# Kernel optimization log

Hardware: AMD Instinct MI355X
Metric: run time of the kernel (lower is better)

Reference implementation:

```python
import jax, jax.numpy as jnp
import numpy as np

B, C, H, W = 256, 512, 14, 14
HW = H * W
TAU = 0.03          # args.tau
EPS = 0.65          # args.epsilon
EPS2 = 0.40         # args.epsilon - args.epsilon_margin
T_LOGIT = 0.07      # args.logit_temperature
MAX_ITERS = 32      # static unrolled bound for the data-dependent while-loop
PD_EPS = 1e-6       # torch.nn.PairwiseDistance default eps (added to the difference)


def setup_inputs() -> dict:
    key = jax.random.key(0)
    k1, k2 = jax.random.split(key)
    img = jax.random.normal(k1, (B, C, H, W), jnp.float32)
    img = img / (jnp.linalg.norm(img, axis=1, keepdims=True) + 1e-12)  # L2 over channels
    aud = jax.random.normal(k2, (B, C), jnp.float32)
    aud = aud / (jnp.linalg.norm(aud, axis=1, keepdims=True) + 1e-12)
    return {"img": img, "aud": aud}


def reference(img, aud):
    Bb, Cc, Hh, Ww = img.shape
    n_pix = Hh * Ww

    # PosLogits: [B,1,H,W]; Alllogits: [B,B,H,W]
    pos_logits = jnp.einsum('ncqa,nc->nqa', img, aud)[:, None]
    all_logits = jnp.einsum('ncqa,kc->nkqa', img, aud)

    # trimap negatives
    pos2 = jax.nn.sigmoid((pos_logits - EPS2) / TAU)
    neg = 1.0 - pos2                                        # [B,1,H,W]

    logit = img.reshape(Bb, Cc, -1) * pos_logits.reshape(Bb, 1, -1)   # [B,C,HW]
    positive0 = pos_logits.reshape(Bb, -1)                            # [B,HW]
    neg_val = (logit * neg.reshape(Bb, 1, -1)).mean(axis=2)           # [B,C]

    logit_t = logit.transpose(0, 2, 1)                                 # [B,HW,C]
    dist_to_zero = jnp.linalg.norm(logit_t - neg_val[:, None, :] + PD_EPS, axis=-1)  # [B,HW]

    def body(t, state):
        positive, already_pos, endpoint, obj = state
        idx = jnp.argmax(positive, axis=1)                             # [B] (detached in torch)
        sel = jnp.take_along_axis(logit, idx[:, None, None], axis=2)[:, :, 0]  # [B,C]
        obj = obj.at[t].set(sel * (~endpoint)[:, None].astype(sel.dtype))
        dist_to_logit = jnp.linalg.norm(logit_t - sel[:, None, :] + PD_EPS, axis=-1)  # [B,HW]
        pos = (dist_to_logit < dist_to_zero) & (~already_pos)
        already_pos = already_pos | pos
        positive = positive * (1.0 - pos.astype(positive.dtype))
        endpoint = endpoint | (pos.sum(axis=1) == 0) | (positive.max(axis=1) < 0.1)
        return (positive, already_pos, endpoint, obj)

    obj0 = jnp.zeros((MAX_ITERS, Bb, Cc), img.dtype)
    state0 = (positive0,
              jnp.zeros((Bb, n_pix), bool),
              jnp.zeros((Bb,), bool),
              obj0)
    _, _, _, object_arr = jax.lax.fori_loop(0, MAX_ITERS, body, state0)

    # lvs contrastive loss
    mask = 1.0 - 100.0 * jnp.eye(Bb, dtype=img.dtype)
    pos_m = jax.nn.sigmoid((pos_logits - EPS) / TAU)                   # [B,1,H,W]
    pos_all = jax.nn.sigmoid((all_logits - EPS) / TAU)                 # [B,B,H,W]
    sim1 = (pos_m * pos_logits).reshape(Bb, 1, -1).sum(-1) / pos_m.reshape(Bb, 1, -1).sum(-1)
    sim = (pos_all * all_logits).reshape(Bb, Bb, -1).sum(-1) / pos_all.reshape(Bb, Bb, -1).sum(-1) * mask
    sim2 = (neg * pos_logits).reshape(Bb, 1, -1).sum(-1) / neg.reshape(Bb, 1, -1).sum(-1)
    logits = jnp.concatenate((sim1, sim, sim2), axis=1) / T_LOGIT      # [B, B+2]
    loss = -jax.nn.log_softmax(logits, axis=1)[:, 0].mean()           # CE with target 0

    return loss, pos_logits[:, 0], object_arr
```

## Files before the change

kernel.cpp:

```cpp
#include <hip/hip_runtime.h>
#include <hip/hip_bf16.h>
#include <math.h>

#define NB 256
#define NC 512
#define NP 196
#define NIT 32
#define PROWS 208
#define LSTR 72
#define SFSTR 211

typedef __attribute__((ext_vector_type(8))) short bf16x8;
typedef __attribute__((ext_vector_type(4))) float f32x4;

__device__ __forceinline__ float sigf(float z){ return 1.0f/(1.0f+expf(-z)); }

__device__ __forceinline__ unsigned short f2bf(float x){
  return __bfloat16_as_ushort(__float2bfloat16(x));
}
__device__ __forceinline__ float bf2f(unsigned short h){
  union{float f; unsigned u;} v; v.u = ((unsigned)h)<<16; return v.f;
}
__device__ __forceinline__ double dshfl_xor(double v, int m){
  int lo = __shfl_xor(__double2loint(v), m);
  int hi = __shfl_xor(__double2hiint(v), m);
  return __hiloint2double(hi, lo);
}

__global__ __launch_bounds__(256) void aud2bf_kernel(const float* __restrict__ aud, unsigned short* __restrict__ aud_bf)
{
  int i = blockIdx.x*256 + threadIdx.x;
  aud_bf[i] = f2bf(aud[i]);
}


__global__ __launch_bounds__(512) void convert5_kernel(
    const float* __restrict__ img, const float* __restrict__ aud,
    unsigned short* __restrict__ pan,
    double* __restrict__ ppl, double* __restrict__ pcs)
{
  const int bid = blockIdx.x;
  const int b = bid & 255, part = bid >> 8;
  const int tid = threadIdx.x;
  const float* imgb = img + (size_t)b*NC*NP + (size_t)part*64*NP;
  __shared__ float sf[64*SFSTR];
  __shared__ float s_aud[64];
  if (tid < 64) s_aud[tid] = aud[b*NC + part*64 + tid];

  for (int j=tid; j<64*49; j+=512){
    int p4 = j % 49, c = j / 49;
    float4 v = *(const float4*)&imgb[(size_t)c*NP + p4*4];
    sf[c*SFSTR + p4*4+0]=v.x; sf[c*SFSTR + p4*4+1]=v.y;
    sf[c*SFSTR + p4*4+2]=v.z; sf[c*SFSTR + p4*4+3]=v.w;
  }
  __syncthreads();

  unsigned short* pp = pan + (size_t)(b*8+part)*PROWS*128;
  for (int j=tid; j<PROWS*8; j+=512){
    int p = j>>3, o = j&7;
    unsigned hw[4], lw[4];
    double dot=0.0, sm=0.0;
    #pragma unroll
    for (int k2=0;k2<4;++k2){
      int c = o*8 + 2*k2;
      float x0 = (p<NP) ? sf[c*SFSTR + p]     : 0.f;
      float x1 = (p<NP) ? sf[(c+1)*SFSTR + p] : 0.f;
      unsigned short h0=f2bf(x0), h1=f2bf(x1);
      unsigned short l0=f2bf(x0-bf2f(h0)), l1=f2bf(x1-bf2f(h1));
      hw[k2] = (unsigned)h0 | ((unsigned)h1<<16);
      lw[k2] = (unsigned)l0 | ((unsigned)l1<<16);
      dot += (double)x0*(double)s_aud[c] + (double)x1*(double)s_aud[c+1];
      sm  += (double)x0 + (double)x1;
    }
    *(uint4*)&pp[p*128 + o*8]      = *(uint4*)hw;
    *(uint4*)&pp[p*128 + 64 + o*8] = *(uint4*)lw;
    dot += dshfl_xor(dot,1); dot += dshfl_xor(dot,2); dot += dshfl_xor(dot,4);
    sm  += dshfl_xor(sm,1);  sm  += dshfl_xor(sm,2);  sm  += dshfl_xor(sm,4);
    if (o==0 && p<NP){
      ppl[(size_t)(b*8+part)*NP + p] = dot;
      pcs[(size_t)(b*8+part)*NP + p] = sm;
    }
  }
}

__global__ __launch_bounds__(256) void prep3_kernel(
    const double* __restrict__ ppl, const double* __restrict__ pcs,
    float* __restrict__ pl, float* __restrict__ cs,
    float* __restrict__ sim1, float* __restrict__ sim2, float* __restrict__ out_pl)
{
  const int b = blockIdx.x, tid = threadIdx.x;
  __shared__ double s_redd[256];
  float plv=0.f;
  if (tid < NP){
    double a=0.0, s=0.0;
    #pragma unroll
    for (int part=0; part<8; ++part){
      a += ppl[(size_t)(b*8+part)*NP + tid];
      s += pcs[(size_t)(b*8+part)*NP + tid];
    }
    plv=(float)a;
    float csv=(float)s;
    pl[b*NP+tid]=plv; cs[b*NP+tid]=csv; out_pl[b*NP+tid]=plv;
  }
  float pmw = (tid<NP)? sigf((plv-0.65f)/0.03f) : 0.f;
  float negw= (tid<NP)? 1.0f - sigf((plv-0.40f)/0.03f) : 0.f;
  double r[4];
  r[0]=(tid<NP)?(double)pmw*(double)plv:0.0;
  r[1]=(tid<NP)?(double)pmw:0.0;
  r[2]=(tid<NP)?(double)negw*(double)plv:0.0;
  r[3]=(tid<NP)?(double)negw:0.0;
  double res[4];
  for (int i=0;i<4;++i){
    __syncthreads();
    s_redd[tid]=r[i];
    __syncthreads();
    for (int s=128;s>0;s>>=1){ if (tid<s) s_redd[tid]+=s_redd[tid+s]; __syncthreads(); }
    res[i]=s_redd[0];
  }
  if (tid==0){
    sim1[b]=(float)(res[0]/res[1]);
    sim2[b]=(float)(res[2]/res[3]);
  }
}

__global__ __launch_bounds__(512) void gram2_kernel(
    const unsigned short* __restrict__ pan, float* __restrict__ G)
{
  const int bid = blockIdx.x;
  const int slot = bid & 7, seq = bid >> 3;
  const int b = slot + 8*(seq>>1), h = seq & 1;
  const int cbase = 7*h, ncl = 7 - h;
  const int tid = threadIdx.x, lane = tid & 63, w = tid >> 6;
  const int nr = (w<5)?2:1;
  const unsigned short* pb = pan + (size_t)b*8*PROWS*128;
  float* Gb = G + (size_t)b*NP*NP;
  __shared__ short smh[PROWS*LSTR];
  __shared__ short sml[PROWS*LSTR];

  f32x4 acc[2][7];
  #pragma unroll
  for (int i=0;i<2;++i)
    #pragma unroll
    for (int j=0;j<7;++j) acc[i][j]=(f32x4){0,0,0,0};

  for (int sl=0; sl<8; ++sl){
    __syncthreads();
    for (int j=tid; j<PROWS*8; j+=512){
      int p = j>>3, o = j&7;
      const unsigned short* src = pb + ((size_t)sl*PROWS + p)*128;
      *(uint4*)&smh[p*LSTR + o*8] = *(const uint4*)(src + o*8);
      *(uint4*)&sml[p*LSTR + o*8] = *(const uint4*)(src + 64 + o*8);
    }
    __syncthreads();
    #pragma unroll
    for (int kk=0; kk<2; ++kk){
      bf16x8 Ah[2], Al[2];
      #pragma unroll
      for (int i=0;i<2;++i){
        if (i<nr){
          int r = (w + 8*i)*16 + (lane&15);
          Ah[i] = *(const bf16x8*)&smh[r*LSTR + kk*32 + (lane>>4)*8];
          Al[i] = *(const bf16x8*)&sml[r*LSTR + kk*32 + (lane>>4)*8];
        }
      }
      #pragma unroll
      for (int j=0;j<7;++j){
        if (j<ncl){
          int r = (cbase+j)*16 + (lane&15);
          bf16x8 Bh = *(const bf16x8*)&smh[r*LSTR + kk*32 + (lane>>4)*8];
          bf16x8 Bl = *(const bf16x8*)&sml[r*LSTR + kk*32 + (lane>>4)*8];
          #pragma unroll
          for (int i=0;i<2;++i){
            if (i<nr){
              acc[i][j] = __builtin_amdgcn_mfma_f32_16x16x32_bf16(Ah[i], Bh, acc[i][j], 0,0,0);
              acc[i][j] = __builtin_amdgcn_mfma_f32_16x16x32_bf16(Ah[i], Bl, acc[i][j], 0,0,0);
              acc[i][j] = __builtin_amdgcn_mfma_f32_16x16x32_bf16(Al[i], Bh, acc[i][j], 0,0,0);
            }
          }
        }
      }
    }
  }

  const int r0 = (lane>>4)*4, colL = lane & 15;
  #pragma unroll
  for (int i=0;i<2;++i){
    #pragma unroll
    for (int j=0;j<7;++j){
      if (i<nr && j<ncl){
        int row = (w+8*i)*16 + r0;
        int col = (cbase+j)*16 + colL;
        if (col < NP){
          #pragma unroll
          for (int jj=0;jj<4;++jj){
            if (row+jj < NP) Gb[(size_t)(row+jj)*NP + col] = acc[i][j][jj];
          }
        }
      }
    }
  }
}

__global__ __launch_bounds__(512) void simgemm2_kernel(
    const unsigned short* __restrict__ pan, const unsigned short* __restrict__ aud_bf,
    float* __restrict__ sumWA, float* __restrict__ sumW)
{
  const int bid = blockIdx.x;
  const int slot = bid & 7, seq = bid >> 3;
  const int b = slot + 8*(seq>>1), h = seq & 1;
  const int tid = threadIdx.x, lane = tid & 63, w = tid >> 6;
  const int wr = w >> 2, wc = w & 3;
  const int pbase = (wr==0)?0:7, npt = 7-wr;
  const unsigned short* pb = pan + (size_t)b*8*PROWS*128;
  __shared__ short smh[PROWS*LSTR];
  __shared__ short sma[128*LSTR];
  __shared__ float sred[2][2][4][2][16];

  f32x4 acc[7][2];
  #pragma unroll
  for (int i=0;i<7;++i)
    #pragma unroll
    for (int n=0;n<2;++n) acc[i][n]=(f32x4){0,0,0,0};

  for (int sl=0; sl<8; ++sl){
    __syncthreads();
    for (int j=tid; j<PROWS*8; j+=512){
      int p = j>>3, o = j&7;
      *(uint4*)&smh[p*LSTR + o*8] = *(const uint4*)(pb + ((size_t)sl*PROWS + p)*128 + o*8);
    }
    for (int j=tid; j<128*8; j+=512){
      int n = j>>3, o = j&7;
      *(uint4*)&sma[n*LSTR + o*8] = *(const uint4*)(aud_bf + (size_t)(h*128+n)*NC + sl*64 + o*8);
    }
    __syncthreads();
    #pragma unroll
    for (int kk=0; kk<2; ++kk){
      bf16x8 Ah[7];
      #pragma unroll
      for (int i=0;i<7;++i){
        if (i<npt){
          int r = (pbase+i)*16 + (lane&15);
          Ah[i] = *(const bf16x8*)&smh[r*LSTR + kk*32 + (lane>>4)*8];
        }
      }
      #pragma unroll
      for (int n=0;n<2;++n){
        int r = (wc*2+n)*16 + (lane&15);
        bf16x8 Bn = *(const bf16x8*)&sma[r*LSTR + kk*32 + (lane>>4)*8];
        #pragma unroll
        for (int i=0;i<7;++i)
          if (i<npt)
            acc[i][n] = __builtin_amdgcn_mfma_f32_16x16x32_bf16(Ah[i], Bn, acc[i][n], 0,0,0);
      }
    }
  }

  float swa[2]={0,0}, sw[2]={0,0};
  #pragma unroll
  for (int n=0;n<2;++n){
    #pragma unroll
    for (int i=0;i<7;++i){
      if (i<npt){
        int rowbase = (pbase+i)*16 + (lane>>4)*4;
        #pragma unroll
        for (int jj=0;jj<4;++jj){
          if (rowbase+jj < NP){
            float v = acc[i][n][jj];
            float wgt = sigf((v-0.65f)/0.03f);
            swa[n] += wgt*v; sw[n] += wgt;
          }
        }
      }
    }
  }
  #pragma unroll
  for (int n=0;n<2;++n){
    swa[n] += __shfl_xor(swa[n],16); swa[n] += __shfl_xor(swa[n],32);
    sw[n]  += __shfl_xor(sw[n],16);  sw[n]  += __shfl_xor(sw[n],32);
  }
  if (lane < 16){
    #pragma unroll
    for (int n=0;n<2;++n){
      sred[0][wr][wc][n][lane] = swa[n];
      sred[1][wr][wc][n][lane] = sw[n];
    }
  }
  __syncthreads();
  if (tid < 128){
    int wc2 = tid>>5, n2 = (tid>>4)&1, col = tid&15;
    float a = sred[0][0][wc2][n2][col] + sred[0][1][wc2][n2][col];
    float s = sred[1][0][wc2][n2][col] + sred[1][1][wc2][n2][col];
    int kcol = h*128 + (wc2*2+n2)*16 + col;
    sumWA[(size_t)b*NB + kcol] = a;
    sumW [(size_t)b*NB + kcol] = s;
  }
}

__global__ __launch_bounds__(256) void loop3_kernel(
    const float* __restrict__ pl, const float* __restrict__ cs,
    const float* __restrict__ G, int* __restrict__ qseq, int* __restrict__ zf)
{
  const int b = blockIdx.x, tid = threadIdx.x, lane = tid & 63, w = tid >> 6;
  const float* Gb = G + (size_t)b*NP*NP;
  __shared__ float sG[NP*NP];
  __shared__ float s_pl[NP], s_wl[NP], s_csL[NP], s_gd[NP];
  __shared__ double gwd[NP];
  __shared__ double s_redd[256];

  #pragma unroll
  for (int k=0;k<38;++k){
    int j = k*256 + tid;
    if (j < NP*NP/4) ((float4*)sG)[j] = ((const float4*)Gb)[j];
  }
  float negw_t = 0.f;
  if (tid < NP){
    float plv = pl[b*NP+tid];
    float csv = cs[b*NP+tid];
    s_pl[tid] = plv;
    s_csL[tid] = plv*csv;
    negw_t = 1.0f - sigf((plv-0.40f)/0.03f);
    s_wl[tid] = plv*negw_t;
    s_gd[tid] = Gb[(size_t)tid*NP + tid];
  }
  __syncthreads();

  double gw = 0.0;
  if (tid < NP){
    for (int q=0;q<NP;++q) gw += (double)sG[q*NP + tid] * (double)s_wl[q];
    gwd[tid] = gw;
  }
  __syncthreads();
  s_redd[tid] = (tid<NP) ? (double)s_wl[tid]*gw : 0.0;
  __syncthreads();
  for (int st=128;st>0;st>>=1){ if (tid<st) s_redd[tid]+=s_redd[tid+st]; __syncthreads(); }
  const double S2 = s_redd[0];
  __syncthreads();
  s_redd[tid] = (tid<NP) ? (double)negw_t*(double)s_csL[tid] : 0.0;
  __syncthreads();
  for (int st=128;st>0;st>>=1){ if (tid<st) s_redd[tid]+=s_redd[tid+st]; __syncthreads(); }
  const double Swl = s_redd[0];
  __syncthreads();

  if (tid < NP){
    const double e = (double)1e-6f;
    double pld = (double)s_pl[tid];
    double d0sq = pld*pld*(double)s_gd[tid]
                - (2.0/196.0)*pld*gwd[tid]
                + S2/(196.0*196.0)
                + 2.0*e*((double)s_csL[tid] - Swl/196.0)
                + 512.0*e*e;
    if (d0sq < 0.0) d0sq = 0.0;
    gwd[tid] = d0sq;
  }
  __syncthreads();

  if (w != 0) return;

  float plv[4], csL[4], gdd[4], posv[4];
  double d0sq[4];
  bool alr[4];
  #pragma unroll
  for (int s=0;s<4;++s){
    int p = lane + 64*s;
    bool valid = p < NP;
    plv[s]  = valid ? s_pl[p]  : 0.f;
    csL[s]  = valid ? s_csL[p] : 0.f;
    gdd[s]  = valid ? s_gd[p]  : 0.f;
    d0sq[s] = valid ? gwd[p]   : 0.0;
    posv[s] = valid ? plv[s]   : -INFINITY;
    alr[s] = false;
  }
  bool endp = false;

  for (int t=0;t<NIT;++t){
    float v = posv[0]; int ix = lane;
    #pragma unroll
    for (int s=1;s<4;++s){
      if (posv[s] > v){ v = posv[s]; ix = lane + 64*s; }
    }
    #pragma unroll
    for (int m=1;m<64;m<<=1){
      float vv = __shfl_xor(v, m);
      int   ii = __shfl_xor(ix, m);
      if (vv>v || (vv==v && ii<ix)){ v=vv; ix=ii; }
    }
    const int q = ix;
    const float plq  = s_pl[q];
    const float gqq  = s_gd[q];
    const float csLq = s_csL[q];
    if (lane==0){ qseq[b*NIT+t] = q; zf[b*NIT+t] = endp ? 1 : 0; }

    int cnt = 0;
    #pragma unroll
    for (int s=0;s<4;++s){
      int p = lane + 64*s;
      if (p<NP && !alr[s]){
        float Gpq = sG[q*NP + p];
        double plp=(double)plv[s], dq=(double)plq;
        const double e=(double)1e-6f;
        double d2 = plp*plp*(double)gdd[s]
                  - 2.0*plp*dq*(double)Gpq
                  + dq*dq*(double)gqq
                  + 2.0*e*((double)csL[s]-(double)csLq)
                  + 512.0*e*e;
        if (d2<0.0) d2=0.0;
        if (d2 < d0sq[s]){ alr[s]=true; posv[s]=posv[s]*0.0f; cnt++; }
      }
    }
    float mx = fmaxf(fmaxf(posv[0],posv[1]),fmaxf(posv[2],posv[3]));
    #pragma unroll
    for (int m=1;m<64;m<<=1){
      cnt += __shfl_xor(cnt, m);
      mx = fmaxf(mx, __shfl_xor(mx, m));
    }
    if (cnt==0 || mx<0.1f) endp=true;
  }
}

__global__ __launch_bounds__(64) void objw_kernel(
    const unsigned short* __restrict__ pan,
    const float* __restrict__ pl, const int* __restrict__ qseq, const int* __restrict__ zf,
    float* __restrict__ obj)
{
  const int bid = blockIdx.x;
  const int b = bid >> 5, t = bid & 31;
  const int lane = threadIdx.x;
  float* op = obj + ((size_t)t*NB + b)*NC;
  const int z = zf[b*NIT + t];
  if (z){
    float4 zv = {0.f,0.f,0.f,0.f};
    *(float4*)&op[lane*8]   = zv;
    *(float4*)&op[lane*8+4] = zv;
    return;
  }
  const int q = qseq[b*NIT + t];
  const float plq = pl[b*NP + q];
  const int part = lane >> 3, off = lane & 7;
  const unsigned short* src = pan + ((size_t)(b*8+part)*PROWS + q)*128;
  uint4 hv = *(const uint4*)(src + off*8);
  uint4 lv = *(const uint4*)(src + 64 + off*8);
  const unsigned* hw = (const unsigned*)&hv;
  const unsigned* lw = (const unsigned*)&lv;
  float o8[8];
  #pragma unroll
  for (int k2=0;k2<4;++k2){
    float x0 = bf2f((unsigned short)(hw[k2]&0xffff)) + bf2f((unsigned short)(lw[k2]&0xffff));
    float x1 = bf2f((unsigned short)(hw[k2]>>16))    + bf2f((unsigned short)(lw[k2]>>16));
    o8[2*k2]   = x0*plq;
    o8[2*k2+1] = x1*plq;
  }
  *(float4*)&op[lane*8]   = *(float4*)&o8[0];
  *(float4*)&op[lane*8+4] = *(float4*)&o8[4];
}

__global__ __launch_bounds__(256) void finalize_b(
    const float* __restrict__ sim1, const float* __restrict__ sim2,
    const float* __restrict__ sumWA, const float* __restrict__ sumW,
    float* __restrict__ lossb)
{
  const int b = blockIdx.x, k = threadIdx.x;
  __shared__ float s_red[256];
  __shared__ double s_redd[256];
  const float T = 0.07f;
  float s = sumWA[(size_t)b*NB+k]/sumW[(size_t)b*NB+k];
  if (k==b) s *= -99.0f;
  const float lk = s/T;
  const float l0 = sim1[b]/T, ll = sim2[b]/T;
  s_red[k]=lk; __syncthreads();
  for (int st=128;st>0;st>>=1){ if(k<st) s_red[k]=fmaxf(s_red[k],s_red[k+st]); __syncthreads(); }
  const float m = fmaxf(s_red[0], fmaxf(l0,ll));
  __syncthreads();
  double e = (double)expf(lk-m);
  if (k==0) e += (double)expf(l0-m)+(double)expf(ll-m);
  s_redd[k]=e; __syncthreads();
  for (int st=128;st>0;st>>=1){ if(k<st) s_redd[k]+=s_redd[k+st]; __syncthreads(); }
  if (k==0) lossb[b] = -(float)((double)(l0-m) - log(s_redd[0]));
}

__global__ __launch_bounds__(256) void finalize_sum(const float* __restrict__ lossb, float* __restrict__ out_loss)
{
  const int tid = threadIdx.x;
  __shared__ double sr[256];
  sr[tid]=(double)lossb[tid]; __syncthreads();
  for (int st=128;st>0;st>>=1){ if(tid<st) sr[tid]+=sr[tid+st]; __syncthreads(); }
  if (tid==0) out_loss[0]=(float)(sr[0]/256.0);
}

extern "C" void kernel_launch(void* const* d_in, const int* in_sizes, int n_in,
                              void* d_out, int out_size, void* d_ws, size_t ws_size,
                              hipStream_t stream)
{
  const float* img = (const float*)d_in[0];
  const float* aud = (const float*)d_in[1];
  float* out = (float*)d_out;
  float* ws  = (float*)d_ws;

  float* pl    = ws;
  float* cs    = pl    + NB*NP;
  float* sim1  = cs    + NB*NP;
  float* sim2  = sim1  + NB;
  float* sumWA = sim2  + NB;
  float* sumW  = sumWA + NB*NB;
  unsigned short* aud_bf = (unsigned short*)(sumW + NB*NB);
  float* G     = (float*)(aud_bf + NB*NC);
  unsigned short* pan = (unsigned short*)(G + (size_t)NB*NP*NP);
  int* qseq    = (int*)(pan + (size_t)NB*8*PROWS*128);
  int* zf      = qseq + NB*NIT;
  float* lossb = (float*)(zf + NB*NIT);

  double* ppl = (double*)G;
  double* pcs = ppl + (size_t)NB*8*NP;

  float* out_loss = out;
  float* out_pl   = out + 1;
  float* out_obj  = out + 1 + NB*NP;

  hipLaunchKernelGGL(aud2bf_kernel,   dim3(NB*NC/256), dim3(256), 0, stream, aud, aud_bf);
  hipLaunchKernelGGL(convert5_kernel, dim3(NB*8),      dim3(512), 0, stream, img, aud, pan, ppl, pcs);
  hipLaunchKernelGGL(prep3_kernel,    dim3(NB),        dim3(256), 0, stream, ppl, pcs, pl, cs, sim1, sim2, out_pl);
  hipLaunchKernelGGL(gram2_kernel,    dim3(NB*2),      dim3(512), 0, stream, pan, G);
  hipLaunchKernelGGL(loop3_kernel,    dim3(NB),        dim3(256), 0, stream, pl, cs, G, qseq, zf);
  hipLaunchKernelGGL(simgemm2_kernel, dim3(NB*2),      dim3(512), 0, stream, pan, aud_bf, sumWA, sumW);
  hipLaunchKernelGGL(objw_kernel,     dim3(NB*NIT),    dim3(64),  0, stream, pan, pl, qseq, zf, out_obj);
  hipLaunchKernelGGL(finalize_b,      dim3(NB),        dim3(256), 0, stream, sim1, sim2, sumWA, sumW, lossb);
  hipLaunchKernelGGL(finalize_sum,    dim3(1),         dim3(256), 0, stream, lossb, out_loss);
}
```

Measured before the change: 204.2 us.

## Split hi/lo bf16 planes and widen the greedy loop kernel to 1024 threads

The interleaved hi/lo bf16 panel is split into two separate planes, so simgemm reads only the hi plane it needs and gram and objw read each plane contiguously. Padded rows are no longer written, and the block-to-batch mapping is simplified to a linear one. The loop kernel now runs 1024 threads: the G·w matvec is split across four threads per pixel, and the tree reductions use wavefront shuffles. This is meant to cut bandwidth and speed up the serial preamble. In exchange, the padded rows are left uninitialised, and the larger blocks may lower occupancy.

After: 200.2 us. 1.02x faster.

```diff
diff --git a/kernel.cpp b/kernel.cpp
--- a/kernel.cpp
+++ b/kernel.cpp
@@ -34,9 +34,9 @@
 }
 
 
-__global__ __launch_bounds__(512) void convert5_kernel(
+__global__ __launch_bounds__(512) void convert4_kernel(
     const float* __restrict__ img, const float* __restrict__ aud,
-    unsigned short* __restrict__ pan,
+    unsigned short* __restrict__ hiT, unsigned short* __restrict__ loT,
     double* __restrict__ ppl, double* __restrict__ pcs)
 {
   const int bid = blockIdx.x;
@@ -55,7 +55,8 @@
   }
   __syncthreads();
 
-  unsigned short* pp = pan + (size_t)(b*8+part)*PROWS*128;
+  unsigned short* hp = hiT + (size_t)(b*8+part)*PROWS*64;
+  unsigned short* lp = loT + (size_t)(b*8+part)*PROWS*64;
   for (int j=tid; j<PROWS*8; j+=512){
     int p = j>>3, o = j&7;
     unsigned hw[4], lw[4];
@@ -72,8 +73,10 @@
       dot += (double)x0*(double)s_aud[c] + (double)x1*(double)s_aud[c+1];
       sm  += (double)x0 + (double)x1;
     }
-    *(uint4*)&pp[p*128 + o*8]      = *(uint4*)hw;
-    *(uint4*)&pp[p*128 + 64 + o*8] = *(uint4*)lw;
+    if (p < NP){
+      *(uint4*)&hp[p*64 + o*8] = *(uint4*)hw;
+      *(uint4*)&lp[p*64 + o*8] = *(uint4*)lw;
+    }
     dot += dshfl_xor(dot,1); dot += dshfl_xor(dot,2); dot += dshfl_xor(dot,4);
     sm  += dshfl_xor(sm,1);  sm  += dshfl_xor(sm,2);  sm  += dshfl_xor(sm,4);
     if (o==0 && p<NP){
@@ -124,15 +127,16 @@
 }
 
 __global__ __launch_bounds__(512) void gram2_kernel(
-    const unsigned short* __restrict__ pan, float* __restrict__ G)
+    const unsigned short* __restrict__ hiT, const unsigned short* __restrict__ loT,
+    float* __restrict__ G)
 {
   const int bid = blockIdx.x;
-  const int slot = bid & 7, seq = bid >> 3;
-  const int b = slot + 8*(seq>>1), h = seq & 1;
+  const int b = bid & 255, h = bid >> 8;
   const int cbase = 7*h, ncl = 7 - h;
   const int tid = threadIdx.x, lane = tid & 63, w = tid >> 6;
   const int nr = (w<5)?2:1;
-  const unsigned short* pb = pan + (size_t)b*8*PROWS*128;
+  const unsigned short* hb = hiT + (size_t)b*8*PROWS*64;
+  const unsigned short* lb = loT + (size_t)b*8*PROWS*64;
   float* Gb = G + (size_t)b*NP*NP;
   __shared__ short smh[PROWS*LSTR];
   __shared__ short sml[PROWS*LSTR];
@@ -147,9 +151,9 @@
     __syncthreads();
     for (int j=tid; j<PROWS*8; j+=512){
       int p = j>>3, o = j&7;
-      const unsigned short* src = pb + ((size_t)sl*PROWS + p)*128;
-      *(uint4*)&smh[p*LSTR + o*8] = *(const uint4*)(src + o*8);
-      *(uint4*)&sml[p*LSTR + o*8] = *(const uint4*)(src + 64 + o*8);
+      size_t src = ((size_t)sl*PROWS + p)*64 + o*8;
+      *(uint4*)&smh[p*LSTR + o*8] = *(const uint4*)(hb + src);
+      *(uint4*)&sml[p*LSTR + o*8] = *(const uint4*)(lb + src);
     }
     __syncthreads();
     #pragma unroll
@@ -202,16 +206,15 @@
 }
 
 __global__ __launch_bounds__(512) void simgemm2_kernel(
-    const unsigned short* __restrict__ pan, const unsigned short* __restrict__ aud_bf,
+    const unsigned short* __restrict__ hiT, const unsigned short* __restrict__ aud_bf,
     float* __restrict__ sumWA, float* __restrict__ sumW)
 {
   const int bid = blockIdx.x;
-  const int slot = bid & 7, seq = bid >> 3;
-  const int b = slot + 8*(seq>>1), h = seq & 1;
+  const int b = bid & 255, h = bid >> 8;
   const int tid = threadIdx.x, lane = tid & 63, w = tid >> 6;
   const int wr = w >> 2, wc = w & 3;
   const int pbase = (wr==0)?0:7, npt = 7-wr;
-  const unsigned short* pb = pan + (size_t)b*8*PROWS*128;
+  const unsigned short* hb = hiT + (size_t)b*8*PROWS*64;
   __shared__ short smh[PROWS*LSTR];
   __shared__ short sma[128*LSTR];
   __shared__ float sred[2][2][4][2][16];
@@ -226,7 +229,7 @@
     __syncthreads();
     for (int j=tid; j<PROWS*8; j+=512){
       int p = j>>3, o = j&7;
-      *(uint4*)&smh[p*LSTR + o*8] = *(const uint4*)(pb + ((size_t)sl*PROWS + p)*128 + o*8);
+      *(uint4*)&smh[p*LSTR + o*8] = *(const uint4*)(hb + ((size_t)sl*PROWS + p)*64 + o*8);
     }
     for (int j=tid; j<128*8; j+=512){
       int n = j>>3, o = j&7;
@@ -296,7 +299,7 @@
   }
 }
 
-__global__ __launch_bounds__(256) void loop3_kernel(
+__global__ __launch_bounds__(1024) void loop4_kernel(
     const float* __restrict__ pl, const float* __restrict__ cs,
     const float* __restrict__ G, int* __restrict__ qseq, int* __restrict__ zf)
 {
@@ -305,11 +308,12 @@
   __shared__ float sG[NP*NP];
   __shared__ float s_pl[NP], s_wl[NP], s_csL[NP], s_gd[NP];
   __shared__ double gwd[NP];
-  __shared__ double s_redd[256];
-
-  #pragma unroll
-  for (int k=0;k<38;++k){
-    int j = k*256 + tid;
+  __shared__ double s_wred[16];
+  __shared__ double s_bc;
+
+  #pragma unroll
+  for (int k=0;k<10;++k){
+    int j = k*1024 + tid;
     if (j < NP*NP/4) ((float4*)sG)[j] = ((const float4*)Gb)[j];
   }
   float negw_t = 0.f;
@@ -324,21 +328,35 @@
   }
   __syncthreads();
 
-  double gw = 0.0;
-  if (tid < NP){
-    for (int q=0;q<NP;++q) gw += (double)sG[q*NP + tid] * (double)s_wl[q];
-    gwd[tid] = gw;
-  }
-  __syncthreads();
-  s_redd[tid] = (tid<NP) ? (double)s_wl[tid]*gw : 0.0;
-  __syncthreads();
-  for (int st=128;st>0;st>>=1){ if (tid<st) s_redd[tid]+=s_redd[tid+st]; __syncthreads(); }
-  const double S2 = s_redd[0];
-  __syncthreads();
-  s_redd[tid] = (tid<NP) ? (double)negw_t*(double)s_csL[tid] : 0.0;
-  __syncthreads();
-  for (int st=128;st>0;st>>=1){ if (tid<st) s_redd[tid]+=s_redd[tid+st]; __syncthreads(); }
-  const double Swl = s_redd[0];
+  {
+    int p = tid >> 2, qg = tid & 3;
+    double a = 0.0;
+    if (p < NP){
+      for (int q=qg*49; q<qg*49+49; ++q) a += (double)sG[q*NP + p] * (double)s_wl[q];
+    }
+    a += dshfl_xor(a,1); a += dshfl_xor(a,2);
+    if (qg==0 && p<NP) gwd[p] = a;
+  }
+  __syncthreads();
+
+  double r = (tid<NP) ? (double)s_wl[tid]*gwd[tid] : 0.0;
+  #pragma unroll
+  for (int m=1;m<64;m<<=1) r += dshfl_xor(r,m);
+  if (lane==0) s_wred[w] = r;
+  __syncthreads();
+  if (tid==0){ double t=0.0; for (int i=0;i<16;++i) t += s_wred[i]; s_bc = t; }
+  __syncthreads();
+  const double S2 = s_bc;
+  __syncthreads();
+
+  r = (tid<NP) ? (double)negw_t*(double)s_csL[tid] : 0.0;
+  #pragma unroll
+  for (int m=1;m<64;m<<=1) r += dshfl_xor(r,m);
+  if (lane==0) s_wred[w] = r;
+  __syncthreads();
+  if (tid==0){ double t=0.0; for (int i=0;i<16;++i) t += s_wred[i]; s_bc = t; }
+  __syncthreads();
+  const double Swl = s_bc;
   __syncthreads();
 
   if (tid < NP){
@@ -418,7 +436,7 @@
 }
 
 __global__ __launch_bounds__(64) void objw_kernel(
-    const unsigned short* __restrict__ pan,
+    const unsigned short* __restrict__ hiT, const unsigned short* __restrict__ loT,
     const float* __restrict__ pl, const int* __restrict__ qseq, const int* __restrict__ zf,
     float* __restrict__ obj)
 {
@@ -436,9 +454,9 @@
   const int q = qseq[b*NIT + t];
   const float plq = pl[b*NP + q];
   const int part = lane >> 3, off = lane & 7;
-  const unsigned short* src = pan + ((size_t)(b*8+part)*PROWS + q)*128;
-  uint4 hv = *(const uint4*)(src + off*8);
-  uint4 lv = *(const uint4*)(src + 64 + off*8);
+  size_t src = ((size_t)(b*8+part)*PROWS + q)*64 + off*8;
+  uint4 hv = *(const uint4*)(hiT + src);
+  uint4 lv = *(const uint4*)(loT + src);
   const unsigned* hw = (const unsigned*)&hv;
   const unsigned* lw = (const unsigned*)&lv;
   float o8[8];
@@ -503,8 +521,9 @@
   float* sumW  = sumWA + NB*NB;
   unsigned short* aud_bf = (unsigned short*)(sumW + NB*NB);
   float* G     = (float*)(aud_bf + NB*NC);
-  unsigned short* pan = (unsigned short*)(G + (size_t)NB*NP*NP);
-  int* qseq    = (int*)(pan + (size_t)NB*8*PROWS*128);
+  unsigned short* hiT = (unsigned short*)(G + (size_t)NB*NP*NP);
+  unsigned short* loT = hiT + (size_t)NB*8*PROWS*64;
+  int* qseq    = (int*)(loT + (size_t)NB*8*PROWS*64);
   int* zf      = qseq + NB*NIT;
   float* lossb = (float*)(zf + NB*NIT);
 
@@ -515,13 +534,13 @@
   float* out_pl   = out + 1;
   float* out_obj  = out + 1 + NB*NP;
 
-  hipLaunchKernelGGL(aud2bf_kernel,   dim3(NB*NC/256), dim3(256), 0, stream, aud, aud_bf);
-  hipLaunchKernelGGL(convert5_kernel, dim3(NB*8),      dim3(512), 0, stream, img, aud, pan, ppl, pcs);
-  hipLaunchKernelGGL(prep3_kernel,    dim3(NB),        dim3(256), 0, stream, ppl, pcs, pl, cs, sim1, sim2, out_pl);
-  hipLaunchKernelGGL(gram2_kernel,    dim3(NB*2),      dim3(512), 0, stream, pan, G);
-  hipLaunchKernelGGL(loop3_kernel,    dim3(NB),        dim3(256), 0, stream, pl, cs, G, qseq, zf);
-  hipLaunchKernelGGL(simgemm2_kernel, dim3(NB*2),      dim3(512), 0, stream, pan, aud_bf, sumWA, sumW);
-  hipLaunchKernelGGL(objw_kernel,     dim3(NB*NIT),    dim3(64),  0, stream, pan, pl, qseq, zf, out_obj);
-  hipLaunchKernelGGL(finalize_b,      dim3(NB),        dim3(256), 0, stream, sim1, sim2, sumWA, sumW, lossb);
-  hipLaunchKernelGGL(finalize_sum,    dim3(1),         dim3(256), 0, stream, lossb, out_loss);
-}
+  hipLaunchKernelGGL(aud2bf_kernel,   dim3(NB*NC/256), dim3(256),  0, stream, aud, aud_bf);
+  hipLaunchKernelGGL(convert4_kernel, dim3(NB*8),      dim3(512),  0, stream, img, aud, hiT, loT, ppl, pcs);
+  hipLaunchKernelGGL(prep3_kernel,    dim3(NB),        dim3(256),  0, stream, ppl, pcs, pl, cs, sim1, sim2, out_pl);
+  hipLaunchKernelGGL(gram2_kernel,    dim3(NB*2),      dim3(512),  0, stream, hiT, loT, G);
+  hipLaunchKernelGGL(loop4_kernel,    dim3(NB),        dim3(1024), 0, stream, pl, cs, G, qseq, zf);
+  hipLaunchKernelGGL(simgemm2_kernel, dim3(NB*2),      dim3(512),  0, stream, hiT, aud_bf, sumWA, sumW);
+  hipLaunchKernelGGL(objw_kernel,     dim3(NB*NIT),    dim3(64),   0, stream, hiT, loT, pl, qseq, zf, out_obj);
+  hipLaunchKernelGGL(finalize_b,      dim3(NB),        dim3(256),  0, stream, sim1, sim2, sumWA, sumW, lossb);
+  hipLaunchKernelGGL(finalize_sum,    dim3(1),         dim3(256),  0, stream, lossb, out_loss);
+}
```
